# Performance work log

Measured on AMD Instinct MI355X. Metric: run time of the kernel, lower is better.

## Reference

```python
import jax, jax.numpy as jnp
import numpy as np


def kernel_mus(n_kernels):
    l_mu = [1.0]
    if n_kernels == 1:
        return l_mu
    bin_size = 2.0 / (n_kernels - 1)
    l_mu.append(1 - bin_size / 2)
    for i in range(1, n_kernels - 1):
        l_mu.append(l_mu[i] - bin_size)
    return l_mu


def kernel_sigmas(n_kernels):
    bin_size = 2.0 / (n_kernels - 1)
    l_sigma = [0.0001]
    if n_kernels == 1:
        return l_sigma
    l_sigma += [0.5 * bin_size] * (n_kernels - 1)
    return l_sigma


def setup_inputs() -> dict:
    key = jax.random.key(0)
    k0, k1, k2, k3 = jax.random.split(key, 4)
    B, Q, D, E, V, K = 256, 32, 512, 300, 100000, 11
    query_tokens = jax.random.randint(k0, (B, Q), 0, V)
    doc_tokens = jax.random.randint(k1, (B, D), 0, V)
    emb_table = jax.random.normal(k2, (V, E), jnp.float32) * 0.02
    dense_w = jax.random.uniform(k3, (1, K), jnp.float32, -0.014, 0.014)
    dense_b = jnp.zeros((1,), jnp.float32)
    mu = jnp.asarray(kernel_mus(K), jnp.float32)
    sigma = jnp.asarray(kernel_sigmas(K), jnp.float32)
    return {"query_tokens": query_tokens, "doc_tokens": doc_tokens,
            "emb_table": emb_table, "dense_w": dense_w, "dense_b": dense_b,
            "mu": mu, "sigma": sigma}


def reference(query_tokens, doc_tokens, emb_table, dense_w, dense_b, mu, sigma):
    EPS = 1e-13  # CosineMatrixAttention tiny value
    q_mask = (query_tokens > 0).astype(jnp.float32)   # [B,Q]
    d_mask = (doc_tokens > 0).astype(jnp.float32)     # [B,D]
    q_emb = emb_table[query_tokens]                   # [B,Q,E]
    d_emb = emb_table[doc_tokens]                     # [B,D,E]
    q_n = q_emb / (jnp.linalg.norm(q_emb, axis=-1, keepdims=True) + EPS)
    d_n = d_emb / (jnp.linalg.norm(d_emb, axis=-1, keepdims=True) + EPS)
    cosine = jnp.einsum('bqe,bde->bqd', q_n, d_n)     # [B,Q,D]
    pair_mask = q_mask[:, :, None] * d_mask[:, None, :]  # [B,Q,D]
    cosine_masked = cosine * pair_mask
    # gaussian kernels: [B,Q,D,K]
    diff = cosine_masked[..., None] - mu
    kernels = jnp.exp(-(diff * diff) / (2.0 * sigma * sigma)) * pair_mask[..., None]
    per_kernel_query = jnp.sum(kernels, axis=2)       # [B,Q,K]
    log_pkq = jnp.log(jnp.clip(per_kernel_query, 1e-10)) * 0.01
    log_pkq = log_pkq * q_mask[..., None]
    per_kernel = jnp.sum(log_pkq, axis=1)             # [B,K]
    out = per_kernel @ dense_w.T + dense_b            # [B,1]
    return out[:, 0]
```

## Files before the change

### kernel.cpp

```cpp
#include <hip/hip_runtime.h>


#define B      256
#define BQ     32
#define BD     512
#define EDIM   300
#define KPAD   320
#define NK     11
#define QSTR   328

typedef float floatx4 __attribute__((ext_vector_type(4)));
typedef short shortx8 __attribute__((ext_vector_type(8)));

__device__ __forceinline__ unsigned short f2bf(float f) {
    unsigned int u = __float_as_uint(f);
    return (unsigned short)((u + 0x7fffu + ((u >> 16) & 1u)) >> 16);
}
__device__ __forceinline__ float bf2f(unsigned short h) {
    return __uint_as_float(((unsigned int)h) << 16);
}
__device__ __forceinline__ float sbc(float x) {
    return __uint_as_float(__builtin_amdgcn_readfirstlane(__float_as_uint(x)));
}

__global__ __launch_bounds__(256)
void knrm_norm(const float* __restrict__ emb, unsigned short* __restrict__ ebf,
               float* __restrict__ rnorm, int V)
{
    int r    = blockIdx.x * 16 + (threadIdx.x >> 4);
    int part = threadIdx.x & 15;
    if (r >= V) return;
    const float4* src = (const float4*)(emb + (size_t)r * EDIM);
    uint2*        dst = (uint2*)(ebf + (size_t)r * KPAD);
    float ss = 0.f;
    #pragma unroll
    for (int i = 0; i < 5; ++i) {
        int c = part + i * 16;
        uint2 p = {0u, 0u};
        if (c < EDIM / 4) {
            float4 v = src[c];
            unsigned short h0 = f2bf(v.x), h1 = f2bf(v.y), h2 = f2bf(v.z), h3 = f2bf(v.w);
            p.x = (unsigned int)h0 | ((unsigned int)h1 << 16);
            p.y = (unsigned int)h2 | ((unsigned int)h3 << 16);
            float f0 = bf2f(h0), f1 = bf2f(h1), f2 = bf2f(h2), f3 = bf2f(h3);
            ss += f0 * f0 + f1 * f1 + f2 * f2 + f3 * f3;
        }
        dst[c] = p;
    }
    ss += __shfl_xor(ss, 1);
    ss += __shfl_xor(ss, 2);
    ss += __shfl_xor(ss, 4);
    ss += __shfl_xor(ss, 8);
    if (part == 0) rnorm[r] = 1.f / (sqrtf(ss) + 1e-13f);
}

__device__ __forceinline__ void load_frags(shortx8* bf, const unsigned short* __restrict__ ebf,
                                           int tok, int quad)
{
    const uint4* src = (const uint4*)(ebf + (size_t)tok * KPAD);
    #pragma unroll
    for (int ks = 0; ks < 10; ++ks)
        bf[ks] = *(const shortx8*)&src[quad + ks * 4];
}

__global__ __launch_bounds__(256)
void knrm_main6(const int* __restrict__ qtok, const int* __restrict__ dtok,
                const unsigned short* __restrict__ ebf, const float* __restrict__ rnorm,
                const float* __restrict__ mu, const float* __restrict__ sigma,
                float* __restrict__ pkq_part)
{
    __shared__ unsigned short q_buf[BQ * QSTR];
    __shared__ float pkq_s[BQ * NK];
    __shared__ float rqs[BQ];

    const int tid  = threadIdx.x;
    const int lane = tid & 63;
    const int wv   = tid >> 6;
    const int b    = blockIdx.x & 255;
    const int half = blockIdx.x >> 8;
    const int l16  = lane & 15;
    const int quad = lane >> 4;

    for (int i = tid; i < BQ * NK; i += 256) pkq_s[i] = 0.f;
    if (tid < BQ) rqs[tid] = rnorm[qtok[b * BQ + tid]];

    const int dbase = b * BD + half * 256 + wv * 16 + l16;
    int   td[4];
    float rd[4], dm[4];
    #pragma unroll
    for (int s = 0; s < 4; ++s) {
        td[s] = dtok[dbase + s * 64];
        rd[s] = rnorm[td[s]];
        dm[s] = (td[s] > 0) ? 1.f : 0.f;
    }

    {
        int row = tid >> 3, part = tid & 7;
        int tok = qtok[b * BQ + row];
        const uint4* src = (const uint4*)(ebf + (size_t)tok * KPAD);
        #pragma unroll
        for (int i = 0; i < 5; ++i) {
            int c = part + i * 8;
            *(uint4*)&q_buf[row * QSTR + c * 8] = src[c];
        }
    }

    shortx8 bf0[10], bf1[10];
    load_frags(bf0, ebf, td[0], quad);

    __syncthreads();

    float mur[NK], cfr[NK];
    #pragma unroll
    for (int k = 0; k < NK; ++k) {
        float s = sbc(sigma[k]);
        mur[k] = sbc(mu[k]);
        cfr[k] = -0.5f / (s * s);
    }
    float rqv[8];
    #pragma unroll
    for (int slab = 0; slab < 2; ++slab)
        #pragma unroll
        for (int r = 0; r < 4; ++r)
            rqv[slab * 4 + r] = rqs[slab * 16 + quad * 4 + r];

    const unsigned short* a0 = &q_buf[l16 * QSTR + quad * 8];
    const unsigned short* a1 = a0 + 16 * QSTR;

    float pk[2][4][NK];
    #pragma unroll
    for (int slab = 0; slab < 2; ++slab)
        #pragma unroll
        for (int r = 0; r < 4; ++r)
            #pragma unroll
            for (int k = 0; k < NK; ++k) pk[slab][r][k] = 0.f;

    #pragma unroll
    for (int s = 0; s < 4; ++s) {
        const shortx8* bf = (s & 1) ? bf1 : bf0;

        floatx4 acc0 = {0.f, 0.f, 0.f, 0.f};
        floatx4 acc1 = {0.f, 0.f, 0.f, 0.f};
        #pragma unroll
        for (int ks = 0; ks < 10; ++ks) {
            shortx8 aA = *(const shortx8*)(a0 + ks * 32);
            shortx8 aB = *(const shortx8*)(a1 + ks * 32);
            acc0 = __builtin_amdgcn_mfma_f32_16x16x32_bf16(aA, bf[ks], acc0, 0, 0, 0);
            acc1 = __builtin_amdgcn_mfma_f32_16x16x32_bf16(aB, bf[ks], acc1, 0, 0, 0);
        }

        if (s < 3) load_frags((s & 1) ? bf0 : bf1, ebf, td[s + 1], quad);

        #pragma unroll
        for (int slab = 0; slab < 2; ++slab) {
            floatx4 acc = slab ? acc1 : acc0;
            #pragma unroll
            for (int r = 0; r < 4; ++r) {
                float c0 = acc[r] * rqv[slab * 4 + r] * rd[s];
                #pragma unroll
                for (int k = 0; k < NK; ++k) {
                    float d0 = c0 - mur[k];
                    pk[slab][r][k] += dm[s] * __expf(cfr[k] * d0 * d0);
                }
            }
        }
    }

    #pragma unroll
    for (int slab = 0; slab < 2; ++slab)
        #pragma unroll
        for (int r = 0; r < 4; ++r)
            #pragma unroll
            for (int k = 0; k < NK; ++k) {
                float v = pk[slab][r][k];
                v += __shfl_xor(v, 1);
                v += __shfl_xor(v, 2);
                v += __shfl_xor(v, 4);
                v += __shfl_xor(v, 8);
                if (l16 == 0)
                    atomicAdd(&pkq_s[(slab * 16 + quad * 4 + r) * NK + k], v);
            }
    __syncthreads();

    float* dst = pkq_part + (size_t)(b * 2 + half) * (BQ * NK);
    for (int i = tid; i < BQ * NK; i += 256) dst[i] = pkq_s[i];
}

__global__ __launch_bounds__(64)
void knrm_epi(const int* __restrict__ qtok, const float* __restrict__ dw,
              const float* __restrict__ db, const float* __restrict__ pkq_part,
              float* __restrict__ out)
{
    int b = blockIdx.x, lane = threadIdx.x;
    float sq = 0.f;
    if (lane < BQ) {
        int tok = qtok[b * BQ + lane];
        if (tok > 0) {
            #pragma unroll
            for (int k = 0; k < NK; ++k) {
                float s = pkq_part[((size_t)(b * 2 + 0) * BQ + lane) * NK + k]
                        + pkq_part[((size_t)(b * 2 + 1) * BQ + lane) * NK + k];
                sq += __logf(fmaxf(s, 1e-10f)) * 0.01f * dw[k];
            }
        }
    }
    sq += __shfl_xor(sq, 1);
    sq += __shfl_xor(sq, 2);
    sq += __shfl_xor(sq, 4);
    sq += __shfl_xor(sq, 8);
    sq += __shfl_xor(sq, 16);
    sq += __shfl_xor(sq, 32);
    if (lane == 0) out[b] = sq + db[0];
}

extern "C" void kernel_launch(void* const* d_in, const int* in_sizes, int n_in,
                              void* d_out, int out_size, void* d_ws, size_t ws_size,
                              hipStream_t stream)
{
    const int*   qtok  = (const int*)d_in[0];
    const int*   dtok  = (const int*)d_in[1];
    const float* emb   = (const float*)d_in[2];
    const float* dw    = (const float*)d_in[3];
    const float* dbias = (const float*)d_in[4];
    const float* mu    = (const float*)d_in[5];
    const float* sg    = (const float*)d_in[6];
    float* out = (float*)d_out;

    const int V = in_sizes[2] / EDIM;
    const size_t ebf_bytes = (size_t)V * KPAD * 2;
    const size_t rn_bytes  = (size_t)V * 4;

    unsigned short* ebf = (unsigned short*)d_ws;
    float* rnorm        = (float*)((char*)d_ws + ebf_bytes);
    float* pkq_part     = (float*)((char*)d_ws + ebf_bytes + rn_bytes);

    knrm_norm<<<(V + 15) / 16, 256, 0, stream>>>(emb, ebf, rnorm, V);
    knrm_main6<<<B * 2, 256, 0, stream>>>(qtok, dtok, ebf, rnorm, mu, sg, pkq_part);
    knrm_epi<<<B, 64, 0, stream>>>(qtok, dw, dbias, pkq_part, out);
}
```

Baseline: 231.4 us.

## Fuse epilogue into main kernel with one 512-thread block per batch

The main kernel now runs one 512-thread block per batch row instead of two 256-thread half blocks. This lets the log and dense epilogue be computed in-block from shared memory, removing the partial-sum buffer and the third kernel launch. The norm kernel is also changed so 8 threads handle each row with 16-byte stores instead of 16 threads with 8-byte stores. The trade-off is half as many blocks in the main grid, which may reduce occupancy and latency hiding. The norm pass over the full table likely dominates runtime, so the wider stores there may matter most.

Result: no change. 231.3 us (-0.0%).

```diff
diff --git a/kernel.cpp b/kernel.cpp
--- a/kernel.cpp
+++ b/kernel.cpp
@@ -22,35 +22,44 @@
 __device__ __forceinline__ float sbc(float x) {
     return __uint_as_float(__builtin_amdgcn_readfirstlane(__float_as_uint(x)));
 }
+__device__ __forceinline__ unsigned int pack2(float a, float b, float& ss) {
+    unsigned short h0 = f2bf(a), h1 = f2bf(b);
+    float g0 = bf2f(h0), g1 = bf2f(h1);
+    ss += g0 * g0 + g1 * g1;
+    return (unsigned int)h0 | ((unsigned int)h1 << 16);
+}
 
 __global__ __launch_bounds__(256)
 void knrm_norm(const float* __restrict__ emb, unsigned short* __restrict__ ebf,
                float* __restrict__ rnorm, int V)
 {
-    int r    = blockIdx.x * 16 + (threadIdx.x >> 4);
-    int part = threadIdx.x & 15;
+    int r    = blockIdx.x * 32 + (threadIdx.x >> 3);
+    int part = threadIdx.x & 7;
     if (r >= V) return;
     const float4* src = (const float4*)(emb + (size_t)r * EDIM);
-    uint2*        dst = (uint2*)(ebf + (size_t)r * KPAD);
+    uint4*        dst = (uint4*)(ebf + (size_t)r * KPAD);
     float ss = 0.f;
     #pragma unroll
     for (int i = 0; i < 5; ++i) {
-        int c = part + i * 16;
-        uint2 p = {0u, 0u};
-        if (c < EDIM / 4) {
-            float4 v = src[c];
-            unsigned short h0 = f2bf(v.x), h1 = f2bf(v.y), h2 = f2bf(v.z), h3 = f2bf(v.w);
-            p.x = (unsigned int)h0 | ((unsigned int)h1 << 16);
-            p.y = (unsigned int)h2 | ((unsigned int)h3 << 16);
-            float f0 = bf2f(h0), f1 = bf2f(h1), f2 = bf2f(h2), f3 = bf2f(h3);
-            ss += f0 * f0 + f1 * f1 + f2 * f2 + f3 * f3;
-        }
-        dst[c] = p;
+        int j = part + i * 8;
+        uint4 o = {0u, 0u, 0u, 0u};
+        if (j < 37) {
+            float4 a = src[2 * j];
+            float4 c = src[2 * j + 1];
+            o.x = pack2(a.x, a.y, ss);
+            o.y = pack2(a.z, a.w, ss);
+            o.z = pack2(c.x, c.y, ss);
+            o.w = pack2(c.z, c.w, ss);
+        } else if (j == 37) {
+            float4 a = src[74];
+            o.x = pack2(a.x, a.y, ss);
+            o.y = pack2(a.z, a.w, ss);
+        }
+        dst[j] = o;
     }
     ss += __shfl_xor(ss, 1);
     ss += __shfl_xor(ss, 2);
     ss += __shfl_xor(ss, 4);
-    ss += __shfl_xor(ss, 8);
     if (part == 0) rnorm[r] = 1.f / (sqrtf(ss) + 1e-13f);
 }
 
@@ -63,46 +72,44 @@
         bf[ks] = *(const shortx8*)&src[quad + ks * 4];
 }
 
-__global__ __launch_bounds__(256)
-void knrm_main6(const int* __restrict__ qtok, const int* __restrict__ dtok,
+__global__ __launch_bounds__(512, 2)
+void knrm_main7(const int* __restrict__ qtok, const int* __restrict__ dtok,
                 const unsigned short* __restrict__ ebf, const float* __restrict__ rnorm,
                 const float* __restrict__ mu, const float* __restrict__ sigma,
-                float* __restrict__ pkq_part)
+                const float* __restrict__ dw, const float* __restrict__ db,
+                float* __restrict__ out)
 {
     __shared__ unsigned short q_buf[BQ * QSTR];
     __shared__ float pkq_s[BQ * NK];
     __shared__ float rqs[BQ];
+    __shared__ float red[BQ];
 
     const int tid  = threadIdx.x;
     const int lane = tid & 63;
     const int wv   = tid >> 6;
-    const int b    = blockIdx.x & 255;
-    const int half = blockIdx.x >> 8;
+    const int b    = blockIdx.x;
     const int l16  = lane & 15;
     const int quad = lane >> 4;
 
-    for (int i = tid; i < BQ * NK; i += 256) pkq_s[i] = 0.f;
+    for (int i = tid; i < BQ * NK; i += 512) pkq_s[i] = 0.f;
     if (tid < BQ) rqs[tid] = rnorm[qtok[b * BQ + tid]];
 
-    const int dbase = b * BD + half * 256 + wv * 16 + l16;
+    const int dbase = b * BD + wv * 16 + l16;
     int   td[4];
     float rd[4], dm[4];
     #pragma unroll
     for (int s = 0; s < 4; ++s) {
-        td[s] = dtok[dbase + s * 64];
+        td[s] = dtok[dbase + s * 128];
         rd[s] = rnorm[td[s]];
         dm[s] = (td[s] > 0) ? 1.f : 0.f;
     }
 
     {
-        int row = tid >> 3, part = tid & 7;
+        int row = tid >> 4, part = tid & 15;
         int tok = qtok[b * BQ + row];
-        const uint4* src = (const uint4*)(ebf + (size_t)tok * KPAD);
-        #pragma unroll
-        for (int i = 0; i < 5; ++i) {
-            int c = part + i * 8;
-            *(uint4*)&q_buf[row * QSTR + c * 8] = src[c];
-        }
+        const uint4* src  = (const uint4*)(ebf + (size_t)tok * KPAD);
+        uint4*       qrow = (uint4*)&q_buf[row * QSTR];
+        for (int c = part; c < 40; c += 16) qrow[c] = src[c];
     }
 
     shortx8 bf0[10], bf1[10];
@@ -182,35 +189,25 @@
             }
     __syncthreads();
 
-    float* dst = pkq_part + (size_t)(b * 2 + half) * (BQ * NK);
-    for (int i = tid; i < BQ * NK; i += 256) dst[i] = pkq_s[i];
-}
-
-__global__ __launch_bounds__(64)
-void knrm_epi(const int* __restrict__ qtok, const float* __restrict__ dw,
-              const float* __restrict__ db, const float* __restrict__ pkq_part,
-              float* __restrict__ out)
-{
-    int b = blockIdx.x, lane = threadIdx.x;
-    float sq = 0.f;
-    if (lane < BQ) {
-        int tok = qtok[b * BQ + lane];
+    if (tid < BQ) {
+        int tok = qtok[b * BQ + tid];
+        float sq = 0.f;
         if (tok > 0) {
             #pragma unroll
             for (int k = 0; k < NK; ++k) {
-                float s = pkq_part[((size_t)(b * 2 + 0) * BQ + lane) * NK + k]
-                        + pkq_part[((size_t)(b * 2 + 1) * BQ + lane) * NK + k];
-                sq += __logf(fmaxf(s, 1e-10f)) * 0.01f * dw[k];
+                float s = fmaxf(pkq_s[tid * NK + k], 1e-10f);
+                sq += __logf(s) * 0.01f * dw[k];
             }
         }
-    }
-    sq += __shfl_xor(sq, 1);
-    sq += __shfl_xor(sq, 2);
-    sq += __shfl_xor(sq, 4);
-    sq += __shfl_xor(sq, 8);
-    sq += __shfl_xor(sq, 16);
-    sq += __shfl_xor(sq, 32);
-    if (lane == 0) out[b] = sq + db[0];
+        red[tid] = sq;
+    }
+    __syncthreads();
+    if (tid == 0) {
+        float s = db[0];
+        #pragma unroll 8
+        for (int i = 0; i < BQ; ++i) s += red[i];
+        out[b] = s;
+    }
 }
 
 extern "C" void kernel_launch(void* const* d_in, const int* in_sizes, int n_in,
@@ -228,13 +225,10 @@
 
     const int V = in_sizes[2] / EDIM;
     const size_t ebf_bytes = (size_t)V * KPAD * 2;
-    const size_t rn_bytes  = (size_t)V * 4;
 
     unsigned short* ebf = (unsigned short*)d_ws;
     float* rnorm        = (float*)((char*)d_ws + ebf_bytes);
-    float* pkq_part     = (float*)((char*)d_ws + ebf_bytes + rn_bytes);
-
-    knrm_norm<<<(V + 15) / 16, 256, 0, stream>>>(emb, ebf, rnorm, V);
-    knrm_main6<<<B * 2, 256, 0, stream>>>(qtok, dtok, ebf, rnorm, mu, sg, pkq_part);
-    knrm_epi<<<B, 64, 0, stream>>>(qtok, dw, dbias, pkq_part, out);
-}
+
+    knrm_norm<<<(V + 31) / 32, 256, 0, stream>>>(emb, ebf, rnorm, V);
+    knrm_main7<<<B, 512, 0, stream>>>(qtok, dtok, ebf, rnorm, mu, sg, dw, dbias, out);
+}
```
